# Kernel optimization log

Hardware: AMD Instinct MI355X
Metric: run time of the kernel (lower is better)

Reference implementation:

```python
import jax, jax.numpy as jnp
import numpy as np

B, T, K_LAB = 32, 2048, 256
MASK = 1.0  # scalar mask blend coefficient from __init__ (1.0 = no padding)


def setup_inputs() -> dict:
    key = jax.random.key(0)
    k1, k2, k3 = jax.random.split(key, 3)
    y_pred = jax.random.normal(k1, (B, T, K_LAB), dtype=jnp.float32)  # emissions
    labels = jax.random.randint(k2, (B, T), 0, K_LAB, dtype=jnp.int32)  # gold tag ids
    # crf_trans weight, keras 'uniform' initializer ~ U(-0.05, 0.05)
    trans = jax.random.uniform(k3, (K_LAB, K_LAB), dtype=jnp.float32, minval=-0.05, maxval=0.05)
    return {"y_pred": y_pred, "trans": trans, "labels": labels}


def reference(y_pred, trans, labels):
    K = y_pred.shape[-1]
    y_true = jax.nn.one_hot(labels, K, dtype=y_pred.dtype)  # [B,T,K]

    # ---- path_score (unnormalized log prob of gold path) ----
    point_score = jnp.sum(y_pred * y_true, axis=(1, 2))[:, None]  # [B,1]
    # original materializes [B,T-1,K,K]; einsum computes the same contraction
    trans_score = jnp.einsum('bti,ij,btj->b', y_true[:, :-1], trans, y_true[:, 1:])[:, None]
    path_score = point_score + trans_score  # [B,1]

    # ---- log partition via forward algorithm (log-sum-exp semiring scan) ----
    init = y_pred[:, 0]  # [B,K]

    def step(state, x_t):
        # state: [B,K] alpha_{t-1};  x_t: [B,K] emissions at t
        new = jax.nn.logsumexp(state[:, :, None] + trans[None, :, :], axis=1) + x_t
        new = MASK * new + (1.0 - MASK) * state  # mask blend (identity for MASK=1)
        return new, None

    xs = jnp.swapaxes(y_pred[:, 1:], 0, 1)  # [T-1,B,K]
    final, _ = jax.lax.scan(step, init, xs)
    log_norm = jax.nn.logsumexp(final, axis=1, keepdims=True)  # [B,1]

    return log_norm - path_score  # [B,1] negative log-likelihood
```

## Files before the change

kernel.cpp:

```cpp
#include <hip/hip_runtime.h>

#define B_N 32
#define T_N 2048
#define K_N 256

typedef float f32x4 __attribute__((ext_vector_type(4)));
typedef int i32x8 __attribute__((ext_vector_type(8)));

#define MFMA8(A, B, C) \
  __builtin_amdgcn_mfma_scale_f32_16x16x128_f8f6f4((A), (B), (C), 0, 0, 0, 0x7F7F7F7F, 0, 0x7F7F7F7F)

__global__ __launch_bounds__(256) void k_rowmax(const float* __restrict__ y,
                                                float* __restrict__ mx) {
  int row = blockIdx.x * 4 + (threadIdx.x >> 6);
  int l = threadIdx.x & 63;
  const float4* p = (const float4*)(y + (size_t)row * K_N);
  float4 v = p[l];
  float m = fmaxf(fmaxf(v.x, v.y), fmaxf(v.z, v.w));
#pragma unroll
  for (int s = 1; s < 64; s <<= 1) m = fmaxf(m, __shfl_xor(m, s));
  if (l == 0) mx[row] = m;
}

__global__ __launch_bounds__(256) void k_g8(const float* __restrict__ trans,
                                            unsigned char* __restrict__ GT) {
  int j = blockIdx.x;
  int i = threadIdx.x;
  float g = __expf(trans[i * K_N + j]) - 1.0f;
  int pk = __builtin_amdgcn_cvt_pk_fp8_f32(g, 0.f, 0, false);
  GT[j * K_N + i] = (unsigned char)(pk & 0xff);
}

__global__ __launch_bounds__(256) void k_scores(
    const float* __restrict__ y, const int* __restrict__ lab,
    const float* __restrict__ trans, const float* __restrict__ mx,
    float* __restrict__ smx, float* __restrict__ path) {
  const int b = blockIdx.x;
  const int tid = threadIdx.x;
  float s_mx = 0.f, s_pt = 0.f, s_tr = 0.f;
  for (int t = tid; t < T_N; t += 256) {
    s_mx += mx[b * T_N + t];
    int lt = lab[b * T_N + t];
    s_pt += y[((size_t)b * T_N + t) * K_N + lt];
    if (t < T_N - 1) {
      int lnx = lab[b * T_N + t + 1];
      s_tr += trans[lt * K_N + lnx];
    }
  }
#pragma unroll
  for (int s = 1; s < 64; s <<= 1) {
    s_mx += __shfl_xor(s_mx, s);
    s_pt += __shfl_xor(s_pt, s);
    s_tr += __shfl_xor(s_tr, s);
  }
  __shared__ float r0[4], r1[4], r2[4];
  int w = tid >> 6, l = tid & 63;
  if (l == 0) { r0[w] = s_mx; r1[w] = s_pt; r2[w] = s_tr; }
  __syncthreads();
  if (tid == 0) {
    smx[b] = r0[0] + r0[1] + r0[2] + r0[3];
    path[b] = (r1[0] + r1[1] + r1[2] + r1[3]) + (r2[0] + r2[1] + r2[2] + r2[3]);
  }
}

__global__ __launch_bounds__(256, 1) void k_crf(
    const float* __restrict__ y, const unsigned char* __restrict__ GT,
    const float* __restrict__ mx, const float* __restrict__ smx,
    const float* __restrict__ path, float* __restrict__ out) {
  const int b = blockIdx.x;
  const int tid = threadIdx.x;
  const int w = tid >> 6;
  const int l = tid & 63;
  const int lr = l & 15;
  const int lg = (l >> 4) & 3;

  alignas(64) __shared__ unsigned char vbuf8[2][K_N];
  alignas(16) __shared__ float red2[2][4];

  const float* __restrict__ yb = y + (size_t)b * T_N * K_N + w * 64 + lr;
  const float* __restrict__ mxb = mx + b * T_N;

  i32x8 Bf[4][2];
#pragma unroll
  for (int tt = 0; tt < 4; ++tt) {
#pragma unroll
    for (int h = 0; h < 2; ++h)
      Bf[tt][h] = *(const i32x8*)(GT + (size_t)(w * 64 + tt * 16 + lr) * K_N + h * 128 + lg * 32);
  }

  {
    int c0 = w * 64 + lg * 16 + lr;
    float v0 = __expf(y[(size_t)b * T_N * K_N + c0] - mxb[0]);
    int pk = __builtin_amdgcn_cvt_pk_fp8_f32(v0, 0.f, 0, false);
    vbuf8[0][c0] = (unsigned char)(pk & 0xff);
    float ps = v0;
#pragma unroll
    for (int s = 1; s < 64; s <<= 1) ps += __shfl_xor(ps, s);
    if (l == 0) red2[0][w] = ps;
  }

  float ys[4][4];
  float mxs[4];
#define PREF(P, TT) { int tp_ = (TT); tp_ = tp_ > (T_N - 1) ? (T_N - 1) : tp_; \
    const float* yp_ = yb + (size_t)tp_ * K_N;                                 \
    ys[P][0] = yp_[0];  ys[P][1] = yp_[16];                                    \
    ys[P][2] = yp_[32]; ys[P][3] = yp_[48];                                    \
    mxs[P] = mxb[tp_]; }

  PREF(0, 1) PREF(1, 2) PREF(2, 3) PREF(3, 4)

  float Cn = 0.0f;
  float wv0 = 0.f, wv1 = 0.f, wv2 = 0.f, wv3 = 0.f;

#define BARRIER asm volatile("s_waitcnt lgkmcnt(0)\ns_barrier" ::: "memory");

  BARRIER

#define STEP(TT, P, RB, WB, DO_PREF) {                                         \
    f32x4 r_ = *(const f32x4*)(&red2[((TT) - 1) & 1][0]);                      \
    i32x8 A0_ = *(const i32x8*)(&vbuf8[RB][lg * 32]);                          \
    i32x8 A1_ = *(const i32x8*)(&vbuf8[RB][128 + lg * 32]);                    \
    float Sp_ = (r_[0] + r_[1]) + (r_[2] + r_[3]);                             \
    float ls_ = __logf(Sp_);                                                   \
    float bias_ = mxs[P] + ls_;                                                \
    float e0_ = __expf(ys[P][0] - bias_);                                      \
    float e1_ = __expf(ys[P][1] - bias_);                                      \
    float e2_ = __expf(ys[P][2] - bias_);                                      \
    float e3_ = __expf(ys[P][3] - bias_);                                      \
    if (DO_PREF) PREF(P, (TT) + 4)                                             \
    f32x4 z_ = {0.f, 0.f, 0.f, 0.f};                                           \
    f32x4 a0_ = MFMA8(A1_, Bf[0][1], MFMA8(A0_, Bf[0][0], z_));                \
    f32x4 a1_ = MFMA8(A1_, Bf[1][1], MFMA8(A0_, Bf[1][0], z_));                \
    f32x4 a2_ = MFMA8(A1_, Bf[2][1], MFMA8(A0_, Bf[2][0], z_));                \
    f32x4 a3_ = MFMA8(A1_, Bf[3][1], MFMA8(A0_, Bf[3][0], z_));                \
    wv0 = (Sp_ + a0_[0]) * e0_;                                                \
    wv1 = (Sp_ + a1_[0]) * e1_;                                                \
    wv2 = (Sp_ + a2_[0]) * e2_;                                                \
    wv3 = (Sp_ + a3_[0]) * e3_;                                                \
    Cn += ls_;                                                                 \
    float ps_ = (wv0 + wv1) + (wv2 + wv3);                                     \
    ps_ += __shfl_xor(ps_, 1);                                                 \
    ps_ += __shfl_xor(ps_, 2);                                                 \
    ps_ += __shfl_xor(ps_, 4);                                                 \
    ps_ += __shfl_xor(ps_, 8);                                                 \
    if (l == 0) red2[(TT) & 1][w] = ps_;                                       \
    {                                                                          \
      float sv_ = lg == 0 ? wv0 : lg == 1 ? wv1 : lg == 2 ? wv2 : wv3;         \
      int pk_ = __builtin_amdgcn_cvt_pk_fp8_f32(sv_, 0.f, 0, false);           \
      vbuf8[WB][w * 64 + lg * 16 + lr] = (unsigned char)(pk_ & 0xff);          \
    }                                                                          \
    BARRIER                                                                    \
  }

#pragma unroll 1
  for (int t0 = 1; t0 <= T_N - 7; t0 += 4) {
    STEP(t0,     0, 0, 1, 1)
    STEP(t0 + 1, 1, 1, 0, 1)
    STEP(t0 + 2, 2, 0, 1, 1)
    STEP(t0 + 3, 3, 1, 0, 1)
  }
  STEP(2045, 0, 0, 1, 0)
  STEP(2046, 1, 1, 0, 0)
  STEP(2047, 2, 0, 1, 0)

  if (tid == 0) {
    float S = (red2[1][0] + red2[1][1]) + (red2[1][2] + red2[1][3]);
    out[b] = __logf(S) + Cn + smx[b] - path[b];
  }
}

extern "C" void kernel_launch(void* const* d_in, const int* in_sizes, int n_in,
                              void* d_out, int out_size, void* d_ws, size_t ws_size,
                              hipStream_t stream) {
  const float* y = (const float*)d_in[0];
  const float* trans = (const float*)d_in[1];
  const int* lab = (const int*)d_in[2];
  float* out = (float*)d_out;

  float* mx = (float*)d_ws;
  unsigned char* GT = (unsigned char*)d_ws + (size_t)B_N * T_N * 4;
  float* smx = (float*)((char*)d_ws + (size_t)B_N * T_N * 4 + (size_t)K_N * K_N);
  float* path = smx + B_N;

  k_rowmax<<<dim3(B_N * T_N / 4), dim3(256), 0, stream>>>(y, mx);
  k_g8<<<dim3(K_N), dim3(256), 0, stream>>>(trans, GT);
  k_scores<<<dim3(B_N), dim3(256), 0, stream>>>(y, lab, trans, mx, smx, path);
  k_crf<<<dim3(B_N), dim3(256), 0, stream>>>(y, GT, mx, smx, path, out);
}
```

Measured before the change: 1.134 ms.

## Compute row-sum via MFMA with ones, power-of-two rescale, merge prep kernels

The per-step cross-wave partial-sum reduction (shuffles plus LDS red2 exchange) is replaced by an extra pair of MFMAs against an all-ones FP8 B operand, so every lane gets the full alpha sum directly. The log normalizer becomes an exponent-only power-of-two rescale, accumulated as integer exponents, which drops a logf per step. Each lane now computes one exp instead of four. Rowmax and GT prep are merged into one launch, and the path-score computation moves into the CRF kernel, removing two launches. The cost is two extra MFMAs per step and FP8 summation precision for the normalizer.

```diff
diff --git a/kernel.cpp b/kernel.cpp
--- a/kernel.cpp
+++ b/kernel.cpp
@@ -10,75 +10,62 @@
 #define MFMA8(A, B, C) \
   __builtin_amdgcn_mfma_scale_f32_16x16x128_f8f6f4((A), (B), (C), 0, 0, 0, 0x7F7F7F7F, 0, 0x7F7F7F7F)
 
-__global__ __launch_bounds__(256) void k_rowmax(const float* __restrict__ y,
-                                                float* __restrict__ mx) {
-  int row = blockIdx.x * 4 + (threadIdx.x >> 6);
-  int l = threadIdx.x & 63;
-  const float4* p = (const float4*)(y + (size_t)row * K_N);
-  float4 v = p[l];
-  float m = fmaxf(fmaxf(v.x, v.y), fmaxf(v.z, v.w));
+__global__ __launch_bounds__(256) void k_prep(const float* __restrict__ y,
+                                              float* __restrict__ mx,
+                                              const float* __restrict__ trans,
+                                              unsigned char* __restrict__ GT) {
+  int blk = blockIdx.x;
+  if (blk < B_N * T_N / 4) {
+    int row = blk * 4 + (threadIdx.x >> 6);
+    int l = threadIdx.x & 63;
+    const float4* p = (const float4*)(y + (size_t)row * K_N);
+    float4 v = p[l];
+    float m = fmaxf(fmaxf(v.x, v.y), fmaxf(v.z, v.w));
 #pragma unroll
-  for (int s = 1; s < 64; s <<= 1) m = fmaxf(m, __shfl_xor(m, s));
-  if (l == 0) mx[row] = m;
-}
-
-__global__ __launch_bounds__(256) void k_g8(const float* __restrict__ trans,
-                                            unsigned char* __restrict__ GT) {
-  int j = blockIdx.x;
-  int i = threadIdx.x;
-  float g = __expf(trans[i * K_N + j]) - 1.0f;
-  int pk = __builtin_amdgcn_cvt_pk_fp8_f32(g, 0.f, 0, false);
-  GT[j * K_N + i] = (unsigned char)(pk & 0xff);
-}
-
-__global__ __launch_bounds__(256) void k_scores(
-    const float* __restrict__ y, const int* __restrict__ lab,
-    const float* __restrict__ trans, const float* __restrict__ mx,
-    float* __restrict__ smx, float* __restrict__ path) {
-  const int b = blockIdx.x;
-  const int tid = threadIdx.x;
-  float s_mx = 0.f, s_pt = 0.f, s_tr = 0.f;
-  for (int t = tid; t < T_N; t += 256) {
-    s_mx += mx[b * T_N + t];
-    int lt = lab[b * T_N + t];
-    s_pt += y[((size_t)b * T_N + t) * K_N + lt];
-    if (t < T_N - 1) {
-      int lnx = lab[b * T_N + t + 1];
-      s_tr += trans[lt * K_N + lnx];
-    }
-  }
-#pragma unroll
-  for (int s = 1; s < 64; s <<= 1) {
-    s_mx += __shfl_xor(s_mx, s);
-    s_pt += __shfl_xor(s_pt, s);
-    s_tr += __shfl_xor(s_tr, s);
-  }
-  __shared__ float r0[4], r1[4], r2[4];
-  int w = tid >> 6, l = tid & 63;
-  if (l == 0) { r0[w] = s_mx; r1[w] = s_pt; r2[w] = s_tr; }
-  __syncthreads();
-  if (tid == 0) {
-    smx[b] = r0[0] + r0[1] + r0[2] + r0[3];
-    path[b] = (r1[0] + r1[1] + r1[2] + r1[3]) + (r2[0] + r2[1] + r2[2] + r2[3]);
+    for (int s = 1; s < 64; s <<= 1) m = fmaxf(m, __shfl_xor(m, s));
+    if (l == 0) mx[row] = m;
+  } else {
+    int j = blk - B_N * T_N / 4;
+    int i = threadIdx.x;
+    float g = __expf(trans[i * K_N + j]) - 1.0f;
+    int pk = __builtin_amdgcn_cvt_pk_fp8_f32(g, 0.f, 0, false);
+    GT[j * K_N + i] = (unsigned char)(pk & 0xff);
   }
 }
 
 __global__ __launch_bounds__(256, 1) void k_crf(
     const float* __restrict__ y, const unsigned char* __restrict__ GT,
-    const float* __restrict__ mx, const float* __restrict__ smx,
-    const float* __restrict__ path, float* __restrict__ out) {
+    const float* __restrict__ mx, const int* __restrict__ lab,
+    const float* __restrict__ trans, float* __restrict__ out) {
   const int b = blockIdx.x;
   const int tid = threadIdx.x;
   const int w = tid >> 6;
   const int l = tid & 63;
   const int lr = l & 15;
   const int lg = (l >> 4) & 3;
+  const int mycol = w * 64 + lg * 16 + lr;
 
   alignas(64) __shared__ unsigned char vbuf8[2][K_N];
-  alignas(16) __shared__ float red2[2][4];
+  __shared__ float red[4];
+  __shared__ float pr[8];
 
-  const float* __restrict__ yb = y + (size_t)b * T_N * K_N + w * 64 + lr;
+  const float* __restrict__ ybase = y + (size_t)b * T_N * K_N;
+  const float* __restrict__ ybl = ybase + mycol;
   const float* __restrict__ mxb = mx + b * T_N;
+
+  {
+    float s_pt = 0.f, s_tr = 0.f;
+    const int* lb = lab + b * T_N;
+    for (int t = tid; t < T_N; t += 256) {
+      int lt = lb[t];
+      s_pt += ybase[(size_t)t * K_N + lt];
+      if (t < T_N - 1) s_tr += trans[lt * K_N + lb[t + 1]];
+    }
+    float s_ = s_pt + s_tr;
+#pragma unroll
+    for (int s = 1; s < 64; s <<= 1) s_ += __shfl_xor(s_, s);
+    if (l == 0) pr[w] = s_;
+  }
 
   i32x8 Bf[4][2];
 #pragma unroll
@@ -87,68 +74,61 @@
     for (int h = 0; h < 2; ++h)
       Bf[tt][h] = *(const i32x8*)(GT + (size_t)(w * 64 + tt * 16 + lr) * K_N + h * 128 + lg * 32);
   }
+  i32x8 Bones;
+#pragma unroll
+  for (int q = 0; q < 8; ++q) Bones[q] = 0x38383838;
 
+  float mx0 = mxb[0];
   {
-    int c0 = w * 64 + lg * 16 + lr;
-    float v0 = __expf(y[(size_t)b * T_N * K_N + c0] - mxb[0]);
+    float v0 = __expf(ybl[0] - mx0);
     int pk = __builtin_amdgcn_cvt_pk_fp8_f32(v0, 0.f, 0, false);
-    vbuf8[0][c0] = (unsigned char)(pk & 0xff);
-    float ps = v0;
-#pragma unroll
-    for (int s = 1; s < 64; s <<= 1) ps += __shfl_xor(ps, s);
-    if (l == 0) red2[0][w] = ps;
+    vbuf8[0][mycol] = (unsigned char)(pk & 0xff);
   }
 
-  float ys[4][4];
+  float ys[4];
   float mxs[4];
 #define PREF(P, TT) { int tp_ = (TT); tp_ = tp_ > (T_N - 1) ? (T_N - 1) : tp_; \
-    const float* yp_ = yb + (size_t)tp_ * K_N;                                 \
-    ys[P][0] = yp_[0];  ys[P][1] = yp_[16];                                    \
-    ys[P][2] = yp_[32]; ys[P][3] = yp_[48];                                    \
-    mxs[P] = mxb[tp_]; }
+    ys[P] = ybl[(size_t)tp_ * K_N]; mxs[P] = mxb[tp_]; }
 
   PREF(0, 1) PREF(1, 2) PREF(2, 3) PREF(3, 4)
 
-  float Cn = 0.0f;
-  float wv0 = 0.f, wv1 = 0.f, wv2 = 0.f, wv3 = 0.f;
+  int Eacc = 0;
+  float smx_acc = mx0;
+  float svf = 0.f;
 
 #define BARRIER asm volatile("s_waitcnt lgkmcnt(0)\ns_barrier" ::: "memory");
 
   BARRIER
 
 #define STEP(TT, P, RB, WB, DO_PREF) {                                         \
-    f32x4 r_ = *(const f32x4*)(&red2[((TT) - 1) & 1][0]);                      \
-    i32x8 A0_ = *(const i32x8*)(&vbuf8[RB][lg * 32]);                          \
-    i32x8 A1_ = *(const i32x8*)(&vbuf8[RB][128 + lg * 32]);                    \
-    float Sp_ = (r_[0] + r_[1]) + (r_[2] + r_[3]);                             \
-    float ls_ = __logf(Sp_);                                                   \
-    float bias_ = mxs[P] + ls_;                                                \
-    float e0_ = __expf(ys[P][0] - bias_);                                      \
-    float e1_ = __expf(ys[P][1] - bias_);                                      \
-    float e2_ = __expf(ys[P][2] - bias_);                                      \
-    float e3_ = __expf(ys[P][3] - bias_);                                      \
+    const i32x8* va_ = (const i32x8*)&vbuf8[RB][0];                            \
+    i32x8 A0_ = va_[lg];                                                       \
+    i32x8 A1_ = va_[4 + lg];                                                   \
+    float e_ = __expf(ys[P] - mxs[P]);                                         \
+    smx_acc += mxs[P];                                                         \
     if (DO_PREF) PREF(P, (TT) + 4)                                             \
     f32x4 z_ = {0.f, 0.f, 0.f, 0.f};                                           \
-    f32x4 a0_ = MFMA8(A1_, Bf[0][1], MFMA8(A0_, Bf[0][0], z_));                \
-    f32x4 a1_ = MFMA8(A1_, Bf[1][1], MFMA8(A0_, Bf[1][0], z_));                \
-    f32x4 a2_ = MFMA8(A1_, Bf[2][1], MFMA8(A0_, Bf[2][0], z_));                \
-    f32x4 a3_ = MFMA8(A1_, Bf[3][1], MFMA8(A0_, Bf[3][0], z_));                \
-    wv0 = (Sp_ + a0_[0]) * e0_;                                                \
-    wv1 = (Sp_ + a1_[0]) * e1_;                                                \
-    wv2 = (Sp_ + a2_[0]) * e2_;                                                \
-    wv3 = (Sp_ + a3_[0]) * e3_;                                                \
-    Cn += ls_;                                                                 \
-    float ps_ = (wv0 + wv1) + (wv2 + wv3);                                     \
-    ps_ += __shfl_xor(ps_, 1);                                                 \
-    ps_ += __shfl_xor(ps_, 2);                                                 \
-    ps_ += __shfl_xor(ps_, 4);                                                 \
-    ps_ += __shfl_xor(ps_, 8);                                                 \
-    if (l == 0) red2[(TT) & 1][w] = ps_;                                       \
-    {                                                                          \
-      float sv_ = lg == 0 ? wv0 : lg == 1 ? wv1 : lg == 2 ? wv2 : wv3;         \
-      int pk_ = __builtin_amdgcn_cvt_pk_fp8_f32(sv_, 0.f, 0, false);           \
-      vbuf8[WB][w * 64 + lg * 16 + lr] = (unsigned char)(pk_ & 0xff);          \
-    }                                                                          \
+    f32x4 s0_ = MFMA8(A0_, Bones, z_);                                         \
+    f32x4 s1_ = MFMA8(A1_, Bones, z_);                                         \
+    f32x4 a0l_ = MFMA8(A0_, Bf[0][0], z_);                                     \
+    f32x4 a0h_ = MFMA8(A1_, Bf[0][1], z_);                                     \
+    f32x4 a1l_ = MFMA8(A0_, Bf[1][0], z_);                                     \
+    f32x4 a1h_ = MFMA8(A1_, Bf[1][1], z_);                                     \
+    f32x4 a2l_ = MFMA8(A0_, Bf[2][0], z_);                                     \
+    f32x4 a2h_ = MFMA8(A1_, Bf[2][1], z_);                                     \
+    f32x4 a3l_ = MFMA8(A0_, Bf[3][0], z_);                                     \
+    f32x4 a3h_ = MFMA8(A1_, Bf[3][1], z_);                                     \
+    float Sp_ = s0_[0] + s1_[0];                                               \
+    int sb_ = __float_as_int(Sp_) & 0x7f800000;                                \
+    float rS_ = __int_as_float(0x7F000000 - sb_);                              \
+    Eacc += (sb_ >> 23);                                                       \
+    float er_ = e_ * rS_;                                                      \
+    float ol_ = lg == 0 ? a0l_[0] : lg == 1 ? a1l_[0] : lg == 2 ? a2l_[0] : a3l_[0]; \
+    float oh_ = lg == 0 ? a0h_[0] : lg == 1 ? a1h_[0] : lg == 2 ? a2h_[0] : a3h_[0]; \
+    float wv_ = (Sp_ + (ol_ + oh_)) * er_;                                     \
+    int pk_ = __builtin_amdgcn_cvt_pk_fp8_f32(wv_, 0.f, 0, false);             \
+    vbuf8[WB][mycol] = (unsigned char)(pk_ & 0xff);                            \
+    svf = wv_;                                                                 \
     BARRIER                                                                    \
   }
 
@@ -163,9 +143,18 @@
   STEP(2046, 1, 1, 0, 0)
   STEP(2047, 2, 0, 1, 0)
 
+  {
+    float s = svf;
+#pragma unroll
+    for (int sh = 1; sh < 64; sh <<= 1) s += __shfl_xor(s, sh);
+    if (l == 0) red[w] = s;
+  }
+  BARRIER
   if (tid == 0) {
-    float S = (red2[1][0] + red2[1][1]) + (red2[1][2] + red2[1][3]);
-    out[b] = __logf(S) + Cn + smx[b] - path[b];
+    float S = (red[0] + red[1]) + (red[2] + red[3]);
+    float Cn = (float)(Eacc - 127 * (T_N - 1)) * 0.69314718056f;
+    float path = (pr[0] + pr[1]) + (pr[2] + pr[3]);
+    out[b] = __logf(S) + Cn + smx_acc - path;
   }
 }
 
@@ -179,11 +168,7 @@
 
   float* mx = (float*)d_ws;
   unsigned char* GT = (unsigned char*)d_ws + (size_t)B_N * T_N * 4;
-  float* smx = (float*)((char*)d_ws + (size_t)B_N * T_N * 4 + (size_t)K_N * K_N);
-  float* path = smx + B_N;
 
-  k_rowmax<<<dim3(B_N * T_N / 4), dim3(256), 0, stream>>>(y, mx);
-  k_g8<<<dim3(K_N), dim3(256), 0, stream>>>(trans, GT);
-  k_scores<<<dim3(B_N), dim3(256), 0, stream>>>(y, lab, trans, mx, smx, path);
-  k_crf<<<dim3(B_N), dim3(256), 0, stream>>>(y, GT, mx, smx, path, out);
+  k_prep<<<dim3(B_N * T_N / 4 + K_N), dim3(256), 0, stream>>>(y, mx, trans, GT);
+  k_crf<<<dim3(B_N), dim3(256), 0, stream>>>(y, GT, mx, lab, trans, out);
 }
```

New measurement: 969.7 us. 14.5% less time.
